# Optimization experiments

Hardware: AMD Instinct MI355X
Metric: run time of the kernel (lower is better)

Reference implementation:

```python
import jax, jax.numpy as jnp
import numpy as np

B, L, C = 256, 256, 128
HID, H = 128, 4
D = HID // H            # 32
NUM_LAYERS = 2
NEG_SLOPE = 0.2
LN_EPS = 1e-5


def setup_inputs() -> dict:
    key = jax.random.key(0)
    ks = jax.random.split(key, 16)
    E = 4096
    x = jax.random.normal(ks[0], (B, L, C), dtype=jnp.float32)
    edge_index = jax.random.randint(ks[1], (2, E), 0, C, dtype=jnp.int64)
    s_in = 1.0 / np.sqrt(L)
    s_h = 1.0 / np.sqrt(HID)
    return {
        "x": x,
        "edge_index": edge_index,
        "emb_W": jax.random.normal(ks[2], (L, HID), jnp.float32) * s_in,
        "emb_b": jnp.zeros((HID,), jnp.float32),
        "lin_l_W": jax.random.normal(ks[3], (NUM_LAYERS, HID, HID), jnp.float32) * s_h,
        "lin_l_b": jnp.zeros((NUM_LAYERS, HID), jnp.float32),
        "lin_r_W": jax.random.normal(ks[4], (NUM_LAYERS, HID, HID), jnp.float32) * s_h,
        "lin_r_b": jnp.zeros((NUM_LAYERS, HID), jnp.float32),
        "att": jax.random.normal(ks[5], (NUM_LAYERS, H, D), jnp.float32) * (1.0 / np.sqrt(D)),
        "gat_bias": jnp.zeros((NUM_LAYERS, HID), jnp.float32),
        "ln_gamma": jnp.ones((NUM_LAYERS, HID), jnp.float32),
        "ln_beta": jnp.zeros((NUM_LAYERS, HID), jnp.float32),
        "proj_W": jax.random.normal(ks[6], (HID, L), jnp.float32) * s_h,
        "proj_b": jnp.zeros((L,), jnp.float32),
    }


def _batch_edges(edge_index):
    # replicate single-graph edges per batch sample with node offsets, then add self loops
    E = edge_index.shape[1]
    off = jnp.repeat(jnp.arange(B, dtype=edge_index.dtype) * C, E)
    src = jnp.tile(edge_index[0], B) + off
    dst = jnp.tile(edge_index[1], B) + off
    loop = jnp.arange(B * C, dtype=edge_index.dtype)
    return jnp.concatenate([src, loop]), jnp.concatenate([dst, loop])


def _layer_norm(x, g, b):
    mu = jnp.mean(x, axis=-1, keepdims=True)
    var = jnp.mean(jnp.square(x - mu), axis=-1, keepdims=True)
    return (x - mu) * jax.lax.rsqrt(var + LN_EPS) * g + b


def _gatv2(x, src, dst, Wl, bl, Wr, br, a, bias):
    N = x.shape[0]
    xl = (x @ Wl + bl).reshape(N, H, D)   # source-side transform
    xr = (x @ Wr + br).reshape(N, H, D)   # target-side transform
    e = jax.nn.leaky_relu(xl[src] + xr[dst], NEG_SLOPE)   # (E', H, D)
    logits = jnp.einsum('ehd,hd->eh', e, a)               # (E', H)
    m = jax.ops.segment_max(logits, dst, num_segments=N)
    p = jnp.exp(logits - m[dst])
    s = jax.ops.segment_sum(p, dst, num_segments=N)
    alpha = p / (s[dst] + 1e-16)
    out = jax.ops.segment_sum(xl[src] * alpha[:, :, None], dst, num_segments=N)
    return out.reshape(N, HID) + bias, alpha


def reference(x, edge_index, emb_W, emb_b, lin_l_W, lin_l_b, lin_r_W, lin_r_b,
              att, gat_bias, ln_gamma, ln_beta, proj_W, proj_b):
    src, dst = _batch_edges(edge_index)
    # (B, L, C) -> nodes are channels: (B*C, L) -> embed to HID
    h = x.transpose(0, 2, 1).reshape(B * C, L) @ emb_W + emb_b
    alpha = None
    for i in range(NUM_LAYERS):
        new_h, alpha = _gatv2(h, src, dst, lin_l_W[i], lin_l_b[i],
                              lin_r_W[i], lin_r_b[i], att[i], gat_bias[i])
        new_h = jax.nn.elu(new_h)
        h = h + new_h
        h = _layer_norm(h, ln_gamma[i], ln_beta[i])
        # dropout: eval mode, identity
    # attention map (to_dense_adj semantics: adj[b, src%C, dst%C] = mean_h(alpha), then transpose)
    b_idx = src // C
    dense = jnp.zeros((B, C, C), x.dtype).at[b_idx, src % C, dst % C].add(alpha.mean(axis=-1))
    attn_map = dense.transpose(0, 2, 1)
    out = (h @ proj_W + proj_b).reshape(B, C, L).transpose(0, 2, 1)  # (B, L, C)
    return out, attn_map
```

## Files before the change

### kernel.cpp

```cpp
#include <hip/hip_runtime.h>
#include <hip/hip_fp16.h>
#include <math.h>

#define BB 256
#define LL 256
#define CC 128
#define HIDD 128
#define HH 4
#define DD 32
#define EE 4096
#define NN (BB*CC)
#define LN_EPS 1e-5f

typedef short bf16x8 __attribute__((ext_vector_type(8)));
typedef _Float16 f16x8 __attribute__((ext_vector_type(8)));
typedef float f32x4 __attribute__((ext_vector_type(4)));

__device__ __forceinline__ unsigned bfr(float f) {
    unsigned x = __float_as_uint(f);
    return (x + 0x7FFFu + ((x >> 16) & 1u)) >> 16;
}
__device__ __forceinline__ unsigned pack2(float a, float b) { return bfr(a) | (bfr(b) << 16); }
__device__ __forceinline__ float b2f(unsigned u) { return __uint_as_float(u << 16); }

__device__ __forceinline__ void stage_bf16_rm(ushort* lds, const ushort* src, int ldm, int t) {
    #pragma unroll
    for (int i = 0; i < 8; ++i) {
        int flat = i*256 + t;
        int r = flat >> 4, c = flat & 15;
        uint4 pk = *(const uint4*)(src + (size_t)r*ldm + c*8);
        *(uint4*)&lds[((r*16) + (c ^ (r & 7)))*8] = pk;
    }
}
__device__ __forceinline__ void mfma_tile_128(const ushort* Als, const ushort* Bls,
                                              f32x4 acc[2][8], int w, int lane) {
    int mr = lane & 15, quad = lane >> 4;
    #pragma unroll
    for (int ks = 0; ks < 4; ++ks) {
        int ca = ks*4 + quad;
        bf16x8 a[2], b[8];
        #pragma unroll
        for (int mf = 0; mf < 2; ++mf) {
            int m = w*32 + mf*16 + mr;
            a[mf] = *(const bf16x8*)&Als[((m*16) + (ca ^ (m & 7)))*8];
        }
        #pragma unroll
        for (int nf = 0; nf < 8; ++nf) {
            int n = nf*16 + mr;
            b[nf] = *(const bf16x8*)&Bls[((n*16) + (ca ^ (n & 7)))*8];
        }
        #pragma unroll
        for (int mf = 0; mf < 2; ++mf)
            #pragma unroll
            for (int nf = 0; nf < 8; ++nf)
                acc[mf][nf] = __builtin_amdgcn_mfma_f32_16x16x32_bf16(a[mf], b[nf], acc[mf][nf], 0, 0, 0);
    }
}
#define ZERO_ACC(acc) { _Pragma("unroll") for (int i_=0;i_<2;++i_) { _Pragma("unroll") for (int j_=0;j_<8;++j_) acc[i_][j_] = (f32x4){0.f,0.f,0.f,0.f}; } }

__device__ __forceinline__ void epilogue_to_tile(const __half* __restrict__ xagg,
                                                 const float* __restrict__ gbias,
                                                 const float* __restrict__ ln_g,
                                                 const float* __restrict__ ln_b,
                                                 const float* __restrict__ Sg_b,
                                                 ushort* __restrict__ hmat,
                                                 ushort* __restrict__ tile,
                                                 int b, int t, bool write_h) {
    int nl = t >> 1, fh = t & 1;
    int node = b*CC + nl;
    const __half* xa = xagg + (size_t)node*HIDD + fh*64;
    ushort* hp = hmat + (size_t)node*HIDD + fh*64;
    const float* gb = gbias + fh*64;
    float is0 = Sg_b[(fh*2 + 0)*CC + nl];
    float is1 = Sg_b[(fh*2 + 1)*CC + nl];

    __half2 hv[32];
    float sum = 0.f;
    #pragma unroll
    for (int c = 0; c < 8; ++c) {
        float isv = (c < 4) ? is0 : is1;
        uint4 xu = *(const uint4*)&xa[c*8];
        uint4 hu = *(const uint4*)&hp[c*8];
        const __half2* xp2 = (const __half2*)&xu;
        const ushort* hs = (const ushort*)&hu;
        float gv[8];
        *(float4*)&gv[0] = *(const float4*)&gb[c*8];
        *(float4*)&gv[4] = *(const float4*)&gb[c*8 + 4];
        #pragma unroll
        for (int i = 0; i < 4; ++i) {
            float o0 = __low2float(xp2[i]) * isv + gv[2*i];
            float o1 = __high2float(xp2[i]) * isv + gv[2*i+1];
            o0 = o0 > 0.f ? o0 : (__expf(o0) - 1.f);
            o1 = o1 > 0.f ? o1 : (__expf(o1) - 1.f);
            float v0 = b2f((unsigned)hs[2*i]) + o0;
            float v1 = b2f((unsigned)hs[2*i+1]) + o1;
            sum += v0 + v1;
            hv[c*4 + i] = __floats2half2_rn(v0, v1);
        }
    }
    float mean = (sum + __shfl_xor(sum, 1)) * 0.0078125f;
    float q = 0.f;
    #pragma unroll
    for (int i = 0; i < 32; ++i) {
        float d0 = __low2float(hv[i]) - mean;
        float d1 = __high2float(hv[i]) - mean;
        q += d0*d0 + d1*d1;
    }
    float var = (q + __shfl_xor(q, 1)) * 0.0078125f;
    float rs = rsqrtf(var + LN_EPS);
    const float* lg = ln_g + fh*64;
    const float* lb = ln_b + fh*64;
    #pragma unroll
    for (int c = 0; c < 8; ++c) {
        float gv[8], bv[8];
        *(float4*)&gv[0] = *(const float4*)&lg[c*8];
        *(float4*)&gv[4] = *(const float4*)&lg[c*8 + 4];
        *(float4*)&bv[0] = *(const float4*)&lb[c*8];
        *(float4*)&bv[4] = *(const float4*)&lb[c*8 + 4];
        __align__(16) ushort ov[8];
        #pragma unroll
        for (int i = 0; i < 4; ++i) {
            float d0 = __low2float(hv[c*4 + i]) - mean;
            float d1 = __high2float(hv[c*4 + i]) - mean;
            ov[2*i]   = (ushort)bfr(d0*rs*gv[2*i]   + bv[2*i]);
            ov[2*i+1] = (ushort)bfr(d1*rs*gv[2*i+1] + bv[2*i+1]);
        }
        int cg = fh*8 + c;
        *(uint4*)&tile[((nl*16) + (cg ^ (nl & 7)))*8] = *(uint4*)ov;
        if (write_h) *(uint4*)&hp[c*8] = *(uint4*)ov;
    }
}

__global__ __launch_bounds__(256) void prep_weights(const float* __restrict__ emb_W,
                                                    const float* __restrict__ lWl,
                                                    const float* __restrict__ lWr,
                                                    const float* __restrict__ pW,
                                                    const int* __restrict__ edge,
                                                    ushort* __restrict__ WembT,
                                                    ushort* __restrict__ WlrT,
                                                    ushort* __restrict__ WpT,
                                                    __half* __restrict__ mult_ds) {
    __shared__ int cnt[CC*CC];
    int t = threadIdx.x;
    if (blockIdx.x == 64) {
        for (int i = t; i < CC*CC; i += 256) cnt[i] = 0;
        __syncthreads();
        for (int j = t; j < EE; j += 256) {
            int s = edge[j], d = edge[EE + j];
            atomicAdd(&cnt[s*CC + d], 1);
        }
        __syncthreads();
        for (int o = t; o < CC*CC; o += 256) {
            int dstc = o >> 7, srcc = o & 127;
            int c = cnt[srcc*CC + dstc] + ((srcc == dstc) ? 1 : 0);
            mult_ds[o] = __float2half((float)c);
        }
        return;
    }
    int gid = blockIdx.x * 256 + t;
    float v[8];
    if (gid < 4096) {
        int f = gid >> 5, ch = gid & 31;
        #pragma unroll
        for (int j = 0; j < 8; ++j) v[j] = emb_W[(size_t)(ch*8 + j)*HIDD + f];
        uint4 pk; pk.x = pack2(v[0],v[1]); pk.y = pack2(v[2],v[3]);
        pk.z = pack2(v[4],v[5]); pk.w = pack2(v[6],v[7]);
        *(uint4*)&WembT[(size_t)f*LL + ch*8] = pk;
    } else if (gid < 12288) {
        int g = gid - 4096;
        int mat = g >> 11, f = (g >> 4) & 127, ch = g & 15;
        const float* src = ((mat & 1) ? lWr : lWl) + (size_t)(mat >> 1)*HIDD*HIDD;
        #pragma unroll
        for (int j = 0; j < 8; ++j) v[j] = src[(size_t)(ch*8 + j)*HIDD + f];
        uint4 pk; pk.x = pack2(v[0],v[1]); pk.y = pack2(v[2],v[3]);
        pk.z = pack2(v[4],v[5]); pk.w = pack2(v[6],v[7]);
        *(uint4*)&WlrT[(size_t)mat*HIDD*HIDD + (size_t)f*HIDD + ch*8] = pk;
    } else {
        int g = gid - 12288;
        int l = g >> 4, ch = g & 15;
        #pragma unroll
        for (int j = 0; j < 8; ++j) v[j] = pW[(size_t)(ch*8 + j)*LL + l];
        uint4 pk; pk.x = pack2(v[0],v[1]); pk.y = pack2(v[2],v[3]);
        pk.z = pack2(v[4],v[5]); pk.w = pack2(v[6],v[7]);
        *(uint4*)&WpT[(size_t)l*HIDD + ch*8] = pk;
    }
}

__global__ __launch_bounds__(256) void embed_mfma(const float* __restrict__ x,
                                                  const ushort* __restrict__ WembT,
                                                  const float* __restrict__ bias,
                                                  ushort* __restrict__ hout) {
    __shared__ __align__(16) ushort Als[128*16*8];
    __shared__ __align__(16) ushort Bls[128*16*8];
    int b = blockIdx.x;
    int t = threadIdx.x, lane = t & 63, w = t >> 6;
    f32x4 acc[2][8];
    ZERO_ACC(acc)
    #pragma unroll
    for (int kh = 0; kh < 2; ++kh) {
        if (kh) __syncthreads();
        const float4* x4 = (const float4*)(x + (size_t)b*LL*CC + (size_t)kh*128*CC);
        int rot = (t >> 3) & 3;
        #pragma unroll
        for (int i = 0; i < 8; ++i) {
            int flat = i*256 + t;
            int lp = flat >> 5, c4 = flat & 31;
            float4 v0 = x4[(size_t)(2*lp)*32 + c4];
            float4 v1 = x4[(size_t)(2*lp + 1)*32 + c4];
            int lc = lp >> 2, lh = lp & 3;
            #pragma unroll
            for (int j0 = 0; j0 < 4; ++j0) {
                int j = (j0 + rot) & 3;
                int c = c4*4 + j;
                unsigned pk = pack2(((const float*)&v0)[j], ((const float*)&v1)[j]);
                *(unsigned*)&Als[((c*16) + (lc ^ (c & 7)))*8 + lh*2] = pk;
            }
        }
        stage_bf16_rm(Bls, WembT + kh*128, LL, t);
        __syncthreads();
        mfma_tile_128(Als, Bls, acc, w, lane);
    }
    int mr = lane & 15, quad = lane >> 4;
    #pragma unroll
    for (int nf = 0; nf < 8; ++nf) {
        int f = nf*16 + mr;
        float bv = bias[f];
        #pragma unroll
        for (int mf = 0; mf < 2; ++mf)
            #pragma unroll
            for (int r = 0; r < 4; ++r) {
                int node = w*32 + mf*16 + quad*4 + r;
                hout[((size_t)b*CC + node)*HIDD + f] = (ushort)bfr(acc[mf][nf][r] + bv);
            }
    }
}

__device__ __forceinline__ void lin_body(ushort* Als, ushort* Bls,
                                         const ushort* WlT, const ushort* WrT,
                                         const float* bl, const float* br,
                                         __half* xlT, __half* xrT, int b, int t) {
    int lane = t & 63, w = t >> 6;
    int mr = lane & 15, quad = lane >> 4;
    #pragma unroll
    for (int lr = 0; lr < 2; ++lr) {
        if (lr) __syncthreads();
        stage_bf16_rm(Bls, lr ? WrT : WlT, HIDD, t);
        __syncthreads();
        f32x4 acc[2][8];
        ZERO_ACC(acc)
        mfma_tile_128(Als, Bls, acc, w, lane);
        const float* bias = lr ? br : bl;
        __half* out = lr ? xrT : xlT;
        #pragma unroll
        for (int nf = 0; nf < 8; ++nf) {
            int f = nf*16 + mr;
            float bv = bias[f];
            int h = f >> 5, d = f & 31;
            #pragma unroll
            for (int mf = 0; mf < 2; ++mf)
                #pragma unroll
                for (int r = 0; r < 4; ++r) {
                    int node = w*32 + mf*16 + quad*4 + r;
                    out[(((size_t)b*HH + h)*CC + node)*DD + d] = __float2half(acc[mf][nf][r] + bv);
                }
        }
    }
}

__global__ __launch_bounds__(256) void lin_mfma(const ushort* __restrict__ hmat,
                                                const ushort* __restrict__ WlT,
                                                const ushort* __restrict__ WrT,
                                                const float* __restrict__ bl,
                                                const float* __restrict__ br,
                                                __half* __restrict__ xlT,
                                                __half* __restrict__ xrT) {
    __shared__ __align__(16) ushort Als[128*16*8];
    __shared__ __align__(16) ushort Bls[128*16*8];
    int b = blockIdx.x, t = threadIdx.x;
    stage_bf16_rm(Als, hmat + (size_t)b*CC*HIDD, HIDD, t);
    lin_body(Als, Bls, WlT, WrT, bl, br, xlT, xrT, b, t);
}

__global__ __launch_bounds__(256) void epi_lin(const __half* __restrict__ xagg,
                                               const float* __restrict__ gbias,
                                               const float* __restrict__ ln_g,
                                               const float* __restrict__ ln_b,
                                               const float* __restrict__ Sg,
                                               const ushort* __restrict__ WlT,
                                               const ushort* __restrict__ WrT,
                                               const float* __restrict__ bl,
                                               const float* __restrict__ br,
                                               ushort* __restrict__ hmat,
                                               __half* __restrict__ xlT,
                                               __half* __restrict__ xrT) {
    __shared__ __align__(16) ushort Als[128*16*8];
    __shared__ __align__(16) ushort Bls[128*16*8];
    int b = blockIdx.x, t = threadIdx.x;
    epilogue_to_tile(xagg, gbias, ln_g, ln_b, Sg + (size_t)b*HH*CC, hmat, Als, b, t, true);
    lin_body(Als, Bls, WlT, WrT, bl, br, xlT, xrT, b, t);
}

#define SLOT(q, mr) ((mr)*4 + (((q) ^ (mr) ^ ((mr) >> 2)) & 3))

#define LOGIT_LOOP(FS)                                                        \
    pm0 = -3.0e38f; pm1 = -3.0e38f;                                           \
    _Pragma("unroll")                                                         \
    for (int j = 0; j < 32; ++j) {                                            \
        int src = sg*32 + j;                                                  \
        uint4 R[4];                                                           \
        const uint4* rpt = (const uint4*)&xl_lds[src*DD];                     \
        R[0]=rpt[0]; R[1]=rpt[1]; R[2]=rpt[2]; R[3]=rpt[3];                   \
        float sl = Slq[src];                                                  \
        const __half2* xv = (const __half2*)R;                                \
        __half2 a0 = __floats2half2_rn(0.f,0.f), a1 = a0, a2 = a0, a3 = a0;   \
        _Pragma("unroll")                                                     \
        for (int q = 0; q < 4; ++q) {                                         \
            a0 = __hfma2(qa2[4*q+0], __habs2(__hadd2(xv[4*q+0], xr2[4*q+0])), a0); \
            a1 = __hfma2(qa2[4*q+1], __habs2(__hadd2(xv[4*q+1], xr2[4*q+1])), a1); \
            a2 = __hfma2(qa2[4*q+2], __habs2(__hadd2(xv[4*q+2], xr2[4*q+2])), a2); \
            a3 = __hfma2(qa2[4*q+3], __habs2(__hadd2(xv[4*q+3], xr2[4*q+3])), a3); \
        }                                                                     \
        __half2 ts = __hadd2(__hadd2(a0, a1), __hadd2(a2, a3));               \
        float l = ((FS) + sl) + (__low2float(ts) + __high2float(ts));         \
        if (j & 1) { pm1 = fmaxf(pm1, l); lv[j >> 1] = __floats2half2_rn(lbuf, l); } \
        else       { pm0 = fmaxf(pm0, l); lbuf = l; }                         \
    }

#define EXP_PHASE(DST)                                                        \
    {                                                                         \
        float m_ = fmaxf(fmaxf(rp[0*CC + (DST)], rp[1*CC + (DST)]),           \
                         fmaxf(rp[2*CC + (DST)], rp[3*CC + (DST)]));          \
        uint4 M_[4];                                                          \
        const uint4* mp_ = (const uint4*)(mult_ds + (size_t)(DST)*CC + sg*32);\
        M_[0]=mp_[0]; M_[1]=mp_[1]; M_[2]=mp_[2]; M_[3]=mp_[3];               \
        const __half* mv_ = (const __half*)M_;                                \
        float s0_ = 0.f, s1_ = 0.f;                                           \
        _Pragma("unroll")                                                     \
        for (int i = 0; i < 16; ++i) {                                        \
            float e0 = __expf(__low2float(lv[i]) - m_) * __half2float(mv_[2*i]); \
            float e1 = __expf(__high2float(lv[i]) - m_) * __half2float(mv_[2*i+1]); \
            if (i & 1) s1_ += e0 + e1; else s0_ += e0 + e1;                   \
            lv[i] = __floats2half2_rn(e0, e1);                                \
        }                                                                     \
        sp[sg*CC + (DST)] = s0_ + s1_;                                        \
    }

#define WRITE_P(PF, DST)                                                      \
    {                                                                         \
        int mr_ = dl & 15, dr_ = dl >> 4;                                     \
        __half* pf_ = (PF) + ((size_t)(dr_*4 + sg)*64)*8;                     \
        _Pragma("unroll")                                                     \
        for (int q = 0; q < 4; ++q)                                           \
            *(uint4*)&pf_[SLOT(q, mr_)*8] = *(uint4*)&lv[q*4];                \
        if (Pg) {                                                             \
            __half* pg_ = Pg + (size_t)bh*CC*CC + (size_t)(DST)*CC + sg*32;   \
            _Pragma("unroll")                                                 \
            for (int q = 0; q < 4; ++q)                                       \
                *(uint4*)&pg_[q*8] = *(uint4*)&lv[q*4];                       \
        }                                                                     \
    }

__global__ __launch_bounds__(256)
void gat_fused(const __half* __restrict__ xl_h,
               const __half* __restrict__ xr_h,
               const __half* __restrict__ mult_ds,
               const float* __restrict__ att,
               __half* __restrict__ xagg,
               float* __restrict__ Sg,
               __half* __restrict__ Pg) {
    __shared__ __align__(16) __half smemA[CC*CC];
    __shared__ __align__(16) __half xlT_swz[DD*16*8];
    __half* xl_lds = smemA;
    float*  Slq    = (float*)(smemA + CC*DD);
    float*  rp     = Slq + CC;
    float*  sp     = rp + 4*CC;
    __half* PfragA = smemA + 64*CC;
    __half* PfragB = smemA;

    int bh = blockIdx.x;
    int h = bh & 3, b = bh >> 2;
    int t = threadIdx.x;
    int sg = t >> 6, dl = t & 63;
    int dstA = dl, dstB = dl + 64;

    {
        const uint4* spg = (const uint4*)(xl_h + (size_t)bh * CC * DD);
        uint4* dp = (uint4*)xl_lds;
        dp[t] = spg[t];
        dp[t + 256] = spg[t + 256];
    }
    __half2 qa2[16];
    const float* ag = att + h*DD;
    #pragma unroll
    for (int c = 0; c < 8; ++c) {
        float4 av = *(const float4*)&ag[c*4];
        qa2[2*c+0] = __floats2half2_rn(0.4f*av.x, 0.4f*av.y);
        qa2[2*c+1] = __floats2half2_rn(0.4f*av.z, 0.4f*av.w);
    }
    __half2 xr2[16];
    float fSA;
    {
        uint4 XA[4];
        const uint4* pa = (const uint4*)(xr_h + ((size_t)bh*CC + dstA)*DD);
        #pragma unroll
        for (int c = 0; c < 4; ++c) XA[c] = pa[c];
        const __half2* va = (const __half2*)XA;
        float sA = 0.f;
        #pragma unroll
        for (int i = 0; i < 16; ++i) {
            xr2[i] = va[i];
            __half2 p = __hmul2(qa2[i], xr2[i]);
            sA += __low2float(p) + __high2float(p);
        }
        fSA = 1.5f * sA;
    }
    __syncthreads();

    if (t < CC) {
        uint4 R[4];
        const uint4* rpt = (const uint4*)&xl_lds[t*DD];
        #pragma unroll
        for (int c = 0; c < 4; ++c) R[c] = rpt[c];
        const __half2* rv = (const __half2*)R;
        __half2 s = __floats2half2_rn(0.f, 0.f);
        #pragma unroll
        for (int i = 0; i < 16; ++i) s = __hfma2(qa2[i], rv[i], s);
        Slq[t] = 1.5f * (__low2float(s) + __high2float(s));
    }
    for (int i = t; i < 512; i += 256) {
        int f = i & 31, c = i >> 5;
        __align__(16) __half v[8];
        #pragma unroll
        for (int e = 0; e < 8; ++e) v[e] = xl_lds[(c*8 + e)*DD + f];
        *(uint4*)&xlT_swz[((f*16) + (c ^ (f & 7)))*8] = *(uint4*)v;
    }
    __syncthreads();

    __align__(16) __half2 lv[16];
    float pm0, pm1, lbuf = 0.f;

    LOGIT_LOOP(fSA)
    rp[sg*CC + dstA] = fmaxf(pm0, pm1);
    __syncthreads();
    EXP_PHASE(dstA)
    WRITE_P(PfragA, dstA)

    float fSB;
    {
        uint4 XB[4];
        const uint4* pb = (const uint4*)(xr_h + ((size_t)bh*CC + dstB)*DD);
        #pragma unroll
        for (int c = 0; c < 4; ++c) XB[c] = pb[c];
        const __half2* vb = (const __half2*)XB;
        float sB = 0.f;
        #pragma unroll
        for (int i = 0; i < 16; ++i) {
            xr2[i] = vb[i];
            __half2 p = __hmul2(qa2[i], xr2[i]);
            sB += __low2float(p) + __high2float(p);
        }
        fSB = 1.5f * sB;
    }

    LOGIT_LOOP(fSB)
    rp[sg*CC + dstB] = fmaxf(pm0, pm1);
    __syncthreads();
    EXP_PHASE(dstB)
    __syncthreads();

    if (sg == 0) {
        float isA = 1.f / (((sp[0*CC + dstA] + sp[1*CC + dstA]) +
                            (sp[2*CC + dstA] + sp[3*CC + dstA])) + 1e-16f);
        float isB = 1.f / (((sp[0*CC + dstB] + sp[1*CC + dstB]) +
                            (sp[2*CC + dstB] + sp[3*CC + dstB])) + 1e-16f);
        Sg[(size_t)bh*CC + dstA] = isA;
        Sg[(size_t)bh*CC + dstB] = isB;
    }
    __syncthreads();
    WRITE_P(PfragB, dstB)
    __syncthreads();

    int quad = dl >> 4, mr = dl & 15;
    f16x8 afr[2][4];
    #pragma unroll
    for (int mf = 0; mf < 2; ++mf) {
        int dr0 = sg*2 + mf;
        const __half* base = (dr0 < 4) ? PfragA : PfragB;
        int drl = dr0 & 3;
        #pragma unroll
        for (int ks = 0; ks < 4; ++ks)
            afr[mf][ks] = *(const f16x8*)&base[((drl*4 + ks)*64 + SLOT(quad, mr))*8];
    }
    f32x4 acc[2][2];
    #pragma unroll
    for (int i = 0; i < 2; ++i)
        #pragma unroll
        for (int j = 0; j < 2; ++j) acc[i][j] = (f32x4){0.f,0.f,0.f,0.f};
    #pragma unroll
    for (int ks = 0; ks < 4; ++ks) {
        int ca = ks*4 + quad;
        f16x8 bfr2[2];
        #pragma unroll
        for (int nf = 0; nf < 2; ++nf) {
            int n = nf*16 + mr;
            bfr2[nf] = *(const f16x8*)&xlT_swz[((n*16) + (ca ^ (n & 7)))*8];
        }
        #pragma unroll
        for (int mf = 0; mf < 2; ++mf)
            #pragma unroll
            for (int nf = 0; nf < 2; ++nf)
                acc[mf][nf] = __builtin_amdgcn_mfma_f32_16x16x32_f16(afr[mf][ks], bfr2[nf], acc[mf][nf], 0, 0, 0);
    }
    #pragma unroll
    for (int mf = 0; mf < 2; ++mf)
        #pragma unroll
        for (int nf = 0; nf < 2; ++nf) {
            int f = nf*16 + mr;
            #pragma unroll
            for (int r = 0; r < 4; ++r) {
                int node = sg*32 + mf*16 + quad*4 + r;
                xagg[(((size_t)b*CC + node)*HH + h)*DD + f] = __float2half(acc[mf][nf][r]);
            }
        }
}

__global__ __launch_bounds__(256) void epi_proj(const __half* __restrict__ xagg,
                                                const float* __restrict__ gbias,
                                                const float* __restrict__ ln_g,
                                                const float* __restrict__ ln_b,
                                                const float* __restrict__ Sg,
                                                const __half* __restrict__ Pg,
                                                const ushort* __restrict__ WpT,
                                                const float* __restrict__ pbias,
                                                ushort* __restrict__ hmat,
                                                float* __restrict__ out,
                                                float* __restrict__ attn_out) {
    __shared__ __align__(16) ushort Als[128*16*8];
    __shared__ __align__(16) ushort Bls[128*16*8];
    int b = blockIdx.x, t = threadIdx.x;
    const float* Sg_b = Sg + (size_t)b*HH*CC;
    epilogue_to_tile(xagg, gbias, ln_g, ln_b, Sg_b, hmat, Bls, b, t, false);

    {
        int nl = t >> 1, fh = t & 1;
        int node = b*CC + nl;
        float ish[HH];
        #pragma unroll
        for (int hh = 0; hh < HH; ++hh) ish[hh] = Sg_b[hh*CC + nl];
        #pragma unroll
        for (int c = 0; c < 8; ++c) {
            float a[8] = {0.f,0.f,0.f,0.f,0.f,0.f,0.f,0.f};
            #pragma unroll
            for (int hh = 0; hh < HH; ++hh) {
                uint4 pu = *(const uint4*)&Pg[((size_t)(b*HH + hh)*CC + nl)*CC + fh*64 + c*8];
                const __half2* pv = (const __half2*)&pu;
                #pragma unroll
                for (int i = 0; i < 4; ++i) {
                    a[2*i]   += __low2float(pv[i]) * ish[hh];
                    a[2*i+1] += __high2float(pv[i]) * ish[hh];
                }
            }
            float4 o0, o1;
            o0.x = 0.25f*a[0]; o0.y = 0.25f*a[1]; o0.z = 0.25f*a[2]; o0.w = 0.25f*a[3];
            o1.x = 0.25f*a[4]; o1.y = 0.25f*a[5]; o1.z = 0.25f*a[6]; o1.w = 0.25f*a[7];
            *(float4*)&attn_out[(size_t)node*CC + fh*64 + c*8]     = o0;
            *(float4*)&attn_out[(size_t)node*CC + fh*64 + c*8 + 4] = o1;
        }
    }

    int lane = t & 63, w = t >> 6;
    int mr = lane & 15, quad = lane >> 4;
    #pragma unroll
    for (int half = 0; half < 2; ++half) {
        __syncthreads();
        stage_bf16_rm(Als, WpT + (size_t)half*128*HIDD, HIDD, t);
        __syncthreads();
        f32x4 acc[2][8];
        ZERO_ACC(acc)
        mfma_tile_128(Als, Bls, acc, w, lane);
        #pragma unroll
        for (int nf = 0; nf < 8; ++nf) {
            int c = nf*16 + mr;
            #pragma unroll
            for (int mf = 0; mf < 2; ++mf)
                #pragma unroll
                for (int r = 0; r < 4; ++r) {
                    int l = half*128 + w*32 + mf*16 + quad*4 + r;
                    out[((size_t)b*LL + l)*CC + c] = acc[mf][nf][r] + pbias[l];
                }
        }
    }
}

extern "C" void kernel_launch(void* const* d_in, const int* in_sizes, int n_in,
                              void* d_out, int out_size, void* d_ws, size_t ws_size,
                              hipStream_t stream) {
    const float* x        = (const float*)d_in[0];
    const int*   edge     = (const int*)d_in[1];
    const float* emb_W    = (const float*)d_in[2];
    const float* emb_b    = (const float*)d_in[3];
    const float* lin_l_W  = (const float*)d_in[4];
    const float* lin_l_b  = (const float*)d_in[5];
    const float* lin_r_W  = (const float*)d_in[6];
    const float* lin_r_b  = (const float*)d_in[7];
    const float* att      = (const float*)d_in[8];
    const float* gat_bias = (const float*)d_in[9];
    const float* ln_g     = (const float*)d_in[10];
    const float* ln_b     = (const float*)d_in[11];
    const float* proj_W   = (const float*)d_in[12];
    const float* proj_b   = (const float*)d_in[13];

    ushort* h     = (ushort*)d_ws;
    __half* xl_h  = (__half*)(h + (size_t)NN * HIDD);
    __half* xr_h  = xl_h + (size_t)NN * HIDD;
    __half* xagg  = xr_h + (size_t)NN * HIDD;
    __half* Pg    = xagg + (size_t)NN * HIDD;
    __half* mult_ds = Pg + (size_t)BB * HH * CC * CC;
    float*  Sg    = (float*)(mult_ds + (size_t)CC * CC);
    ushort* WembT = (ushort*)(Sg + (size_t)BB * HH * CC);
    ushort* WlrT  = WembT + (size_t)CC*LL;
    ushort* WpT   = WlrT + (size_t)4*HIDD*HIDD;

    float* out0 = (float*)d_out;
    float* attn = out0 + (size_t)BB * LL * CC;

    prep_weights<<<65, 256, 0, stream>>>(emb_W, lin_l_W, lin_r_W, proj_W, edge,
                                         WembT, WlrT, WpT, mult_ds);
    embed_mfma<<<BB, 256, 0, stream>>>(x, WembT, emb_b, h);
    lin_mfma<<<BB, 256, 0, stream>>>(h, WlrT, WlrT + (size_t)HIDD*HIDD,
                                     lin_l_b, lin_r_b, xl_h, xr_h);
    gat_fused<<<BB*HH, 256, 0, stream>>>(xl_h, xr_h, mult_ds, att, xagg, Sg, nullptr);
    epi_lin<<<BB, 256, 0, stream>>>(xagg, gat_bias, ln_g, ln_b, Sg,
                                    WlrT + (size_t)2*HIDD*HIDD,
                                    WlrT + (size_t)3*HIDD*HIDD,
                                    lin_l_b + HIDD, lin_r_b + HIDD,
                                    h, xl_h, xr_h);
    gat_fused<<<BB*HH, 256, 0, stream>>>(xl_h, xr_h, mult_ds, att + HIDD, xagg, Sg, Pg);
    epi_proj<<<BB, 256, 0, stream>>>(xagg, gat_bias + HIDD, ln_g + HIDD, ln_b + HIDD,
                                     Sg, Pg, WpT, proj_b, h, out0, attn);
}
```

Before: 290.0 us.

## Split embed, linear, and epilogue kernels into two blocks per sample

The per-sample kernels (embed, lin, epi_lin, epi_proj) now launch a 2xB grid. Each block handles 64 nodes, or half of the projection output rows, instead of the whole 128-node sample. This doubles the block count from 256, so all compute units on the device get work and per-block latency drops. In exchange, the weight tiles are staged twice, and epi_proj recomputes the LayerNorm epilogue for all nodes in both halves.

```diff
diff --git a/kernel.cpp b/kernel.cpp
--- a/kernel.cpp
+++ b/kernel.cpp
@@ -23,7 +23,16 @@
 __device__ __forceinline__ unsigned pack2(float a, float b) { return bfr(a) | (bfr(b) << 16); }
 __device__ __forceinline__ float b2f(unsigned u) { return __uint_as_float(u << 16); }
 
-__device__ __forceinline__ void stage_bf16_rm(ushort* lds, const ushort* src, int ldm, int t) {
+__device__ __forceinline__ void stage_a64(ushort* lds, const ushort* src, int ldm, int t) {
+    #pragma unroll
+    for (int i = 0; i < 4; ++i) {
+        int flat = i*256 + t;
+        int r = flat >> 4, c = flat & 15;
+        uint4 pk = *(const uint4*)(src + (size_t)r*ldm + c*8);
+        *(uint4*)&lds[((r*16) + (c ^ (r & 7)))*8] = pk;
+    }
+}
+__device__ __forceinline__ void stage_b128(ushort* lds, const ushort* src, int ldm, int t) {
     #pragma unroll
     for (int i = 0; i < 8; ++i) {
         int flat = i*256 + t;
@@ -32,6 +41,25 @@
         *(uint4*)&lds[((r*16) + (c ^ (r & 7)))*8] = pk;
     }
 }
+__device__ __forceinline__ void mfma_64x128(const ushort* Als, const ushort* Bls,
+                                            f32x4 acc[8], int w, int lane) {
+    int mr = lane & 15, quad = lane >> 4;
+    int m = w*16 + mr;
+    #pragma unroll
+    for (int ks = 0; ks < 4; ++ks) {
+        int ca = ks*4 + quad;
+        bf16x8 a = *(const bf16x8*)&Als[((m*16) + (ca ^ (m & 7)))*8];
+        bf16x8 b[8];
+        #pragma unroll
+        for (int nf = 0; nf < 8; ++nf) {
+            int n = nf*16 + mr;
+            b[nf] = *(const bf16x8*)&Bls[((n*16) + (ca ^ (n & 7)))*8];
+        }
+        #pragma unroll
+        for (int nf = 0; nf < 8; ++nf)
+            acc[nf] = __builtin_amdgcn_mfma_f32_16x16x32_bf16(a, b[nf], acc[nf], 0, 0, 0);
+    }
+}
 __device__ __forceinline__ void mfma_tile_128(const ushort* Als, const ushort* Bls,
                                               f32x4 acc[2][8], int w, int lane) {
     int mr = lane & 15, quad = lane >> 4;
@@ -56,20 +84,96 @@
                 acc[mf][nf] = __builtin_amdgcn_mfma_f32_16x16x32_bf16(a[mf], b[nf], acc[mf][nf], 0, 0, 0);
     }
 }
-#define ZERO_ACC(acc) { _Pragma("unroll") for (int i_=0;i_<2;++i_) { _Pragma("unroll") for (int j_=0;j_<8;++j_) acc[i_][j_] = (f32x4){0.f,0.f,0.f,0.f}; } }
-
-__device__ __forceinline__ void epilogue_to_tile(const __half* __restrict__ xagg,
-                                                 const float* __restrict__ gbias,
-                                                 const float* __restrict__ ln_g,
-                                                 const float* __restrict__ ln_b,
-                                                 const float* __restrict__ Sg_b,
-                                                 ushort* __restrict__ hmat,
-                                                 ushort* __restrict__ tile,
-                                                 int b, int t, bool write_h) {
+#define ZERO_ACC8(acc) { _Pragma("unroll") for (int j_=0;j_<8;++j_) acc[j_] = (f32x4){0.f,0.f,0.f,0.f}; }
+#define ZERO_ACC28(acc) { _Pragma("unroll") for (int i_=0;i_<2;++i_) { _Pragma("unroll") for (int j_=0;j_<8;++j_) acc[i_][j_] = (f32x4){0.f,0.f,0.f,0.f}; } }
+
+__device__ __forceinline__ void epilogue64(const __half* __restrict__ xagg,
+                                           const float* __restrict__ gbias,
+                                           const float* __restrict__ ln_g,
+                                           const float* __restrict__ ln_b,
+                                           const float* __restrict__ Sg_b,
+                                           ushort* __restrict__ hmat,
+                                           ushort* __restrict__ tile,
+                                           int b, int n0, int t, bool write_h) {
+    int nl = t >> 2, fq = t & 3;
+    int node = b*CC + n0 + nl;
+    const __half* xa = xagg + (size_t)node*HIDD + fq*32;
+    ushort* hp = hmat + (size_t)node*HIDD + fq*32;
+    const float* gb = gbias + fq*32;
+    float isv = Sg_b[fq*CC + n0 + nl];
+
+    __half2 hv[16];
+    float sum = 0.f;
+    #pragma unroll
+    for (int c = 0; c < 4; ++c) {
+        uint4 xu = *(const uint4*)&xa[c*8];
+        uint4 hu = *(const uint4*)&hp[c*8];
+        const __half2* xp2 = (const __half2*)&xu;
+        const ushort* hs = (const ushort*)&hu;
+        float gv[8];
+        *(float4*)&gv[0] = *(const float4*)&gb[c*8];
+        *(float4*)&gv[4] = *(const float4*)&gb[c*8 + 4];
+        #pragma unroll
+        for (int i = 0; i < 4; ++i) {
+            float o0 = __low2float(xp2[i]) * isv + gv[2*i];
+            float o1 = __high2float(xp2[i]) * isv + gv[2*i+1];
+            o0 = o0 > 0.f ? o0 : (__expf(o0) - 1.f);
+            o1 = o1 > 0.f ? o1 : (__expf(o1) - 1.f);
+            float v0 = b2f((unsigned)hs[2*i]) + o0;
+            float v1 = b2f((unsigned)hs[2*i+1]) + o1;
+            sum += v0 + v1;
+            hv[c*4 + i] = __floats2half2_rn(v0, v1);
+        }
+    }
+    sum += __shfl_xor(sum, 1);
+    sum += __shfl_xor(sum, 2);
+    float mean = sum * 0.0078125f;
+    float q = 0.f;
+    #pragma unroll
+    for (int i = 0; i < 16; ++i) {
+        float d0 = __low2float(hv[i]) - mean;
+        float d1 = __high2float(hv[i]) - mean;
+        q += d0*d0 + d1*d1;
+    }
+    q += __shfl_xor(q, 1);
+    q += __shfl_xor(q, 2);
+    float var = q * 0.0078125f;
+    float rs = rsqrtf(var + LN_EPS);
+    const float* lg = ln_g + fq*32;
+    const float* lb = ln_b + fq*32;
+    #pragma unroll
+    for (int c = 0; c < 4; ++c) {
+        float gv[8], bv[8];
+        *(float4*)&gv[0] = *(const float4*)&lg[c*8];
+        *(float4*)&gv[4] = *(const float4*)&lg[c*8 + 4];
+        *(float4*)&bv[0] = *(const float4*)&lb[c*8];
+        *(float4*)&bv[4] = *(const float4*)&lb[c*8 + 4];
+        __align__(16) ushort ov[8];
+        #pragma unroll
+        for (int i = 0; i < 4; ++i) {
+            float d0 = __low2float(hv[c*4 + i]) - mean;
+            float d1 = __high2float(hv[c*4 + i]) - mean;
+            ov[2*i]   = (ushort)bfr(d0*rs*gv[2*i]   + bv[2*i]);
+            ov[2*i+1] = (ushort)bfr(d1*rs*gv[2*i+1] + bv[2*i+1]);
+        }
+        int cg = fq*4 + c;
+        *(uint4*)&tile[((nl*16) + (cg ^ (nl & 7)))*8] = *(uint4*)ov;
+        if (write_h) *(uint4*)&hp[c*8] = *(uint4*)ov;
+    }
+}
+
+__device__ __forceinline__ void epilogue128(const __half* __restrict__ xagg,
+                                            const float* __restrict__ gbias,
+                                            const float* __restrict__ ln_g,
+                                            const float* __restrict__ ln_b,
+                                            const float* __restrict__ Sg_b,
+                                            const ushort* __restrict__ hmat,
+                                            ushort* __restrict__ tile,
+                                            int b, int t) {
     int nl = t >> 1, fh = t & 1;
     int node = b*CC + nl;
     const __half* xa = xagg + (size_t)node*HIDD + fh*64;
-    ushort* hp = hmat + (size_t)node*HIDD + fh*64;
+    const ushort* hp = hmat + (size_t)node*HIDD + fh*64;
     const float* gb = gbias + fh*64;
     float is0 = Sg_b[(fh*2 + 0)*CC + nl];
     float is1 = Sg_b[(fh*2 + 1)*CC + nl];
@@ -127,7 +231,6 @@
         }
         int cg = fh*8 + c;
         *(uint4*)&tile[((nl*16) + (cg ^ (nl & 7)))*8] = *(uint4*)ov;
-        if (write_h) *(uint4*)&hp[c*8] = *(uint4*)ov;
     }
 }
 
@@ -190,35 +293,35 @@
                                                   const ushort* __restrict__ WembT,
                                                   const float* __restrict__ bias,
                                                   ushort* __restrict__ hout) {
-    __shared__ __align__(16) ushort Als[128*16*8];
+    __shared__ __align__(16) ushort Als[64*16*8];
     __shared__ __align__(16) ushort Bls[128*16*8];
-    int b = blockIdx.x;
+    int chalf = blockIdx.x, b = blockIdx.y;
     int t = threadIdx.x, lane = t & 63, w = t >> 6;
-    f32x4 acc[2][8];
-    ZERO_ACC(acc)
+    f32x4 acc[8];
+    ZERO_ACC8(acc)
     #pragma unroll
     for (int kh = 0; kh < 2; ++kh) {
         if (kh) __syncthreads();
         const float4* x4 = (const float4*)(x + (size_t)b*LL*CC + (size_t)kh*128*CC);
         int rot = (t >> 3) & 3;
         #pragma unroll
-        for (int i = 0; i < 8; ++i) {
+        for (int i = 0; i < 4; ++i) {
             int flat = i*256 + t;
-            int lp = flat >> 5, c4 = flat & 31;
-            float4 v0 = x4[(size_t)(2*lp)*32 + c4];
-            float4 v1 = x4[(size_t)(2*lp + 1)*32 + c4];
+            int lp = flat >> 4, c4l = flat & 15;
+            float4 v0 = x4[(size_t)(2*lp)*32 + chalf*16 + c4l];
+            float4 v1 = x4[(size_t)(2*lp + 1)*32 + chalf*16 + c4l];
             int lc = lp >> 2, lh = lp & 3;
             #pragma unroll
             for (int j0 = 0; j0 < 4; ++j0) {
                 int j = (j0 + rot) & 3;
-                int c = c4*4 + j;
+                int cl = c4l*4 + j;
                 unsigned pk = pack2(((const float*)&v0)[j], ((const float*)&v1)[j]);
-                *(unsigned*)&Als[((c*16) + (lc ^ (c & 7)))*8 + lh*2] = pk;
+                *(unsigned*)&Als[((cl*16) + (lc ^ (cl & 7)))*8 + lh*2] = pk;
             }
         }
-        stage_bf16_rm(Bls, WembT + kh*128, LL, t);
+        stage_b128(Bls, WembT + kh*128, LL, t);
         __syncthreads();
-        mfma_tile_128(Als, Bls, acc, w, lane);
+        mfma_64x128(Als, Bls, acc, w, lane);
     }
     int mr = lane & 15, quad = lane >> 4;
     #pragma unroll
@@ -226,29 +329,28 @@
         int f = nf*16 + mr;
         float bv = bias[f];
         #pragma unroll
-        for (int mf = 0; mf < 2; ++mf)
-            #pragma unroll
-            for (int r = 0; r < 4; ++r) {
-                int node = w*32 + mf*16 + quad*4 + r;
-                hout[((size_t)b*CC + node)*HIDD + f] = (ushort)bfr(acc[mf][nf][r] + bv);
-            }
-    }
-}
-
-__device__ __forceinline__ void lin_body(ushort* Als, ushort* Bls,
-                                         const ushort* WlT, const ushort* WrT,
-                                         const float* bl, const float* br,
-                                         __half* xlT, __half* xrT, int b, int t) {
+        for (int r = 0; r < 4; ++r) {
+            int node = chalf*64 + w*16 + quad*4 + r;
+            hout[((size_t)b*CC + node)*HIDD + f] = (ushort)bfr(acc[nf][r] + bv);
+        }
+    }
+}
+
+__device__ __forceinline__ void lin_body64(ushort* Als, ushort* Bls,
+                                           const ushort* WlT, const ushort* WrT,
+                                           const float* bl, const float* br,
+                                           __half* xlT, __half* xrT,
+                                           int b, int n0, int t) {
     int lane = t & 63, w = t >> 6;
     int mr = lane & 15, quad = lane >> 4;
     #pragma unroll
     for (int lr = 0; lr < 2; ++lr) {
         if (lr) __syncthreads();
-        stage_bf16_rm(Bls, lr ? WrT : WlT, HIDD, t);
+        stage_b128(Bls, lr ? WrT : WlT, HIDD, t);
         __syncthreads();
-        f32x4 acc[2][8];
-        ZERO_ACC(acc)
-        mfma_tile_128(Als, Bls, acc, w, lane);
+        f32x4 acc[8];
+        ZERO_ACC8(acc)
+        mfma_64x128(Als, Bls, acc, w, lane);
         const float* bias = lr ? br : bl;
         __half* out = lr ? xrT : xlT;
         #pragma unroll
@@ -257,12 +359,10 @@
             float bv = bias[f];
             int h = f >> 5, d = f & 31;
             #pragma unroll
-            for (int mf = 0; mf < 2; ++mf)
-                #pragma unroll
-                for (int r = 0; r < 4; ++r) {
-                    int node = w*32 + mf*16 + quad*4 + r;
-                    out[(((size_t)b*HH + h)*CC + node)*DD + d] = __float2half(acc[mf][nf][r] + bv);
-                }
+            for (int r = 0; r < 4; ++r) {
+                int node = n0 + w*16 + quad*4 + r;
+                out[(((size_t)b*HH + h)*CC + node)*DD + d] = __float2half(acc[nf][r] + bv);
+            }
         }
     }
 }
@@ -274,11 +374,12 @@
                                                 const float* __restrict__ br,
                                                 __half* __restrict__ xlT,
                                                 __half* __restrict__ xrT) {
-    __shared__ __align__(16) ushort Als[128*16*8];
+    __shared__ __align__(16) ushort Als[64*16*8];
     __shared__ __align__(16) ushort Bls[128*16*8];
-    int b = blockIdx.x, t = threadIdx.x;
-    stage_bf16_rm(Als, hmat + (size_t)b*CC*HIDD, HIDD, t);
-    lin_body(Als, Bls, WlT, WrT, bl, br, xlT, xrT, b, t);
+    int n0 = blockIdx.x * 64, b = blockIdx.y;
+    int t = threadIdx.x;
+    stage_a64(Als, hmat + ((size_t)b*CC + n0)*HIDD, HIDD, t);
+    lin_body64(Als, Bls, WlT, WrT, bl, br, xlT, xrT, b, n0, t);
 }
 
 __global__ __launch_bounds__(256) void epi_lin(const __half* __restrict__ xagg,
@@ -293,11 +394,12 @@
                                                ushort* __restrict__ hmat,
                                                __half* __restrict__ xlT,
                                                __half* __restrict__ xrT) {
-    __shared__ __align__(16) ushort Als[128*16*8];
+    __shared__ __align__(16) ushort Als[64*16*8];
     __shared__ __align__(16) ushort Bls[128*16*8];
-    int b = blockIdx.x, t = threadIdx.x;
-    epilogue_to_tile(xagg, gbias, ln_g, ln_b, Sg + (size_t)b*HH*CC, hmat, Als, b, t, true);
-    lin_body(Als, Bls, WlT, WrT, bl, br, xlT, xrT, b, t);
+    int n0 = blockIdx.x * 64, b = blockIdx.y;
+    int t = threadIdx.x;
+    epilogue64(xagg, gbias, ln_g, ln_b, Sg + (size_t)b*HH*CC, hmat, Als, b, n0, t, true);
+    lin_body64(Als, Bls, WlT, WrT, bl, br, xlT, xrT, b, n0, t);
 }
 
 #define SLOT(q, mr) ((mr)*4 + (((q) ^ (mr) ^ ((mr) >> 2)) & 3))
@@ -532,16 +634,17 @@
                                                 const __half* __restrict__ Pg,
                                                 const ushort* __restrict__ WpT,
                                                 const float* __restrict__ pbias,
-                                                ushort* __restrict__ hmat,
+                                                const ushort* __restrict__ hmat,
                                                 float* __restrict__ out,
                                                 float* __restrict__ attn_out) {
     __shared__ __align__(16) ushort Als[128*16*8];
     __shared__ __align__(16) ushort Bls[128*16*8];
-    int b = blockIdx.x, t = threadIdx.x;
+    int lhalf = blockIdx.x, b = blockIdx.y;
+    int t = threadIdx.x;
     const float* Sg_b = Sg + (size_t)b*HH*CC;
-    epilogue_to_tile(xagg, gbias, ln_g, ln_b, Sg_b, hmat, Bls, b, t, false);
-
-    {
+    epilogue128(xagg, gbias, ln_g, ln_b, Sg_b, hmat, Bls, b, t);
+
+    if (lhalf == 0) {
         int nl = t >> 1, fh = t & 1;
         int node = b*CC + nl;
         float ish[HH];
@@ -570,25 +673,21 @@
 
     int lane = t & 63, w = t >> 6;
     int mr = lane & 15, quad = lane >> 4;
-    #pragma unroll
-    for (int half = 0; half < 2; ++half) {
-        __syncthreads();
-        stage_bf16_rm(Als, WpT + (size_t)half*128*HIDD, HIDD, t);
-        __syncthreads();
-        f32x4 acc[2][8];
-        ZERO_ACC(acc)
-        mfma_tile_128(Als, Bls, acc, w, lane);
-        #pragma unroll
-        for (int nf = 0; nf < 8; ++nf) {
-            int c = nf*16 + mr;
+    stage_b128(Als, WpT + (size_t)lhalf*128*HIDD, HIDD, t);
+    __syncthreads();
+    f32x4 acc[2][8];
+    ZERO_ACC28(acc)
+    mfma_tile_128(Als, Bls, acc, w, lane);
+    #pragma unroll
+    for (int nf = 0; nf < 8; ++nf) {
+        int c = nf*16 + mr;
+        #pragma unroll
+        for (int mf = 0; mf < 2; ++mf)
             #pragma unroll
-            for (int mf = 0; mf < 2; ++mf)
-                #pragma unroll
-                for (int r = 0; r < 4; ++r) {
-                    int l = half*128 + w*32 + mf*16 + quad*4 + r;
-                    out[((size_t)b*LL + l)*CC + c] = acc[mf][nf][r] + pbias[l];
-                }
-        }
+            for (int r = 0; r < 4; ++r) {
+                int l = lhalf*128 + w*32 + mf*16 + quad*4 + r;
+                out[((size_t)b*LL + l)*CC + c] = acc[mf][nf][r] + pbias[l];
+            }
     }
 }
 
@@ -626,16 +725,16 @@
 
     prep_weights<<<65, 256, 0, stream>>>(emb_W, lin_l_W, lin_r_W, proj_W, edge,
                                          WembT, WlrT, WpT, mult_ds);
-    embed_mfma<<<BB, 256, 0, stream>>>(x, WembT, emb_b, h);
-    lin_mfma<<<BB, 256, 0, stream>>>(h, WlrT, WlrT + (size_t)HIDD*HIDD,
-                                     lin_l_b, lin_r_b, xl_h, xr_h);
+    embed_mfma<<<dim3(2, BB), 256, 0, stream>>>(x, WembT, emb_b, h);
+    lin_mfma<<<dim3(2, BB), 256, 0, stream>>>(h, WlrT, WlrT + (size_t)HIDD*HIDD,
+                                              lin_l_b, lin_r_b, xl_h, xr_h);
     gat_fused<<<BB*HH, 256, 0, stream>>>(xl_h, xr_h, mult_ds, att, xagg, Sg, nullptr);
-    epi_lin<<<BB, 256, 0, stream>>>(xagg, gat_bias, ln_g, ln_b, Sg,
-                                    WlrT + (size_t)2*HIDD*HIDD,
-                                    WlrT + (size_t)3*HIDD*HIDD,
-                                    lin_l_b + HIDD, lin_r_b + HIDD,
-                                    h, xl_h, xr_h);
+    epi_lin<<<dim3(2, BB), 256, 0, stream>>>(xagg, gat_bias, ln_g, ln_b, Sg,
+                                             WlrT + (size_t)2*HIDD*HIDD,
+                                             WlrT + (size_t)3*HIDD*HIDD,
+                                             lin_l_b + HIDD, lin_r_b + HIDD,
+                                             h, xl_h, xr_h);
     gat_fused<<<BB*HH, 256, 0, stream>>>(xl_h, xr_h, mult_ds, att + HIDD, xagg, Sg, Pg);
-    epi_proj<<<BB, 256, 0, stream>>>(xagg, gat_bias + HIDD, ln_g + HIDD, ln_b + HIDD,
-                                     Sg, Pg, WpT, proj_b, h, out0, attn);
-}
+    epi_proj<<<dim3(2, BB), 256, 0, stream>>>(xagg, gat_bias + HIDD, ln_g + HIDD, ln_b + HIDD,
+                                              Sg, Pg, WpT, proj_b, h, out0, attn);
+}
```

Result: slower. 306.0 us (+5.5%).
